# Kernel optimization log

Measured on AMD Instinct MI355X. Metric: run time of the kernel, lower is better.

## Reference

```python
import jax, jax.numpy as jnp
import numpy as np

NUM_HEADS = 4
NUM_GROUPS = 32
EPS = 1e-5


def group_norm(x, gamma, beta):
    B, C, H, W = x.shape
    g = x.reshape(B, NUM_GROUPS, C // NUM_GROUPS, H, W)
    mean = g.mean(axis=(2, 3, 4), keepdims=True)
    var = g.var(axis=(2, 3, 4), keepdims=True)
    g = (g - mean) * jax.lax.rsqrt(var + EPS)
    x = g.reshape(B, C, H, W)
    return x * gamma[None, :, None, None] + beta[None, :, None, None]


def setup_inputs() -> dict:
    key = jax.random.key(0)
    ks = jax.random.split(key, 7)
    B, C, H, W = 16, 256, 32, 32
    x = jax.random.normal(ks[0], (B, C, H, W), dtype=jnp.float32)
    gn_gamma = jnp.ones((C,), dtype=jnp.float32)
    gn_beta = jnp.zeros((C,), dtype=jnp.float32)
    s = 1.0 / np.sqrt(C)
    qkv_w = jax.random.normal(ks[1], (3 * C, C), dtype=jnp.float32) * s
    qkv_b = jnp.zeros((3 * C,), dtype=jnp.float32)
    proj_w = jax.random.normal(ks[2], (C, C), dtype=jnp.float32) * s
    proj_b = jnp.zeros((C,), dtype=jnp.float32)
    return {"x": x, "gn_gamma": gn_gamma, "gn_beta": gn_beta,
            "qkv_w": qkv_w, "qkv_b": qkv_b, "proj_w": proj_w, "proj_b": proj_b}


def reference(x, gn_gamma, gn_beta, qkv_w, qkv_b, proj_w, proj_b):
    B, C, H, W = x.shape
    nh = NUM_HEADS
    d = C // nh
    N = H * W

    h = group_norm(x, gn_gamma, gn_beta)
    # 1x1 conv == channel matmul
    qkv = jnp.einsum('bchw,oc->bohw', h, qkv_w) + qkv_b[None, :, None, None]
    qkv = qkv.reshape(B, 3, nh, d, N)
    q, k, v = qkv[:, 0], qkv[:, 1], qkv[:, 2]  # each [B, nh, d, N]

    scale = 1.0 / jnp.sqrt(jnp.asarray(d, dtype=x.dtype))
    attn = jnp.einsum('bhdn,bhdm->bhnm', q, k) * scale  # [B, nh, N, N]
    attn = jax.nn.softmax(attn, axis=-1)
    out = jnp.einsum('bhnm,bhdm->bhdn', attn, v)  # [B, nh, d, N]
    out = out.reshape(B, C, H, W)

    out = jnp.einsum('bchw,oc->bohw', out, proj_w) + proj_b[None, :, None, None]
    return x + out
```

## Files before the change

kernel.cpp:

```cpp
#include <hip/hip_runtime.h>
#include <math.h>

typedef unsigned short u16;
typedef unsigned int u32;
typedef __attribute__((ext_vector_type(8))) short s16x8;
typedef __attribute__((ext_vector_type(4))) float f32x4;

#define NB 16
#define NN 1024
#define GN_EPS 1e-5f

static __device__ __forceinline__ u16 f2bf(float f) {
    union { float f; u32 u; } v; v.f = f;
    return (u16)((v.u + 0x8000u) >> 16);
}
static __device__ __forceinline__ u32 pk2(float a, float b) {
    union { float f; u32 u; } A, B; A.f = a; B.f = b;
    return __builtin_amdgcn_perm(A.u + 0x8000u, B.u + 0x8000u, 0x03020706u);
}
static __device__ __forceinline__ u32 cvtpk2(float a, float b) {
    u32 r;
    asm("v_cvt_pk_bf16_f32 %0, %1, %2" : "=v"(r) : "v"(a), "v"(b));
    return r;
}

#define GLL16(gp, lp) __builtin_amdgcn_global_load_lds( \
    (const __attribute__((address_space(1))) void*)(const void*)(gp), \
    (__attribute__((address_space(3))) void*)(void*)(lp), 16, 0, 0)

__global__ __launch_bounds__(256) void gn_stats_kernel(
    const float* __restrict__ x, float2* __restrict__ stats)
{
    const int bg = blockIdx.x;
    const int t  = threadIdx.x;
    const float4* xb = (const float4*)(x + (size_t)bg * 8192);
    float s = 0.f, ss = 0.f;
#pragma unroll
    for (int i = 0; i < 8; ++i) {
        float4 f = xb[t + i * 256];
        s  += f.x + f.y + f.z + f.w;
        ss += f.x * f.x + f.y * f.y + f.z * f.z + f.w * f.w;
    }
#pragma unroll
    for (int off = 32; off > 0; off >>= 1) {
        s  += __shfl_down(s, off);
        ss += __shfl_down(ss, off);
    }
    __shared__ float red[8];
    const int wid = t >> 6;
    if ((t & 63) == 0) { red[wid] = s; red[4 + wid] = ss; }
    __syncthreads();
    if (t == 0) {
        float sa = red[0] + red[1] + red[2] + red[3];
        float sb = red[4] + red[5] + red[6] + red[7];
        float mean = sa * (1.0f / 8192.0f);
        float var  = sb * (1.0f / 8192.0f) - mean * mean;
        stats[bg] = make_float2(mean, 1.0f / sqrtf(var + GN_EPS));
    }
}

__global__ __launch_bounds__(256) void wcvt_kernel(
    const float* __restrict__ qkv_w, const float* __restrict__ proj_w,
    u16* __restrict__ wqb, u16* __restrict__ wpb)
{
    int i = blockIdx.x * 256 + threadIdx.x;
    if (i < 49152) {
        float4 f = ((const float4*)qkv_w)[i];
        *(uint2*)(wqb + (size_t)i * 4) = make_uint2(pk2(f.x, f.y), pk2(f.z, f.w));
    } else {
        int j = i - 49152;
        float4 f = ((const float4*)proj_w)[j];
        *(uint2*)(wpb + (size_t)j * 4) = make_uint2(pk2(f.x, f.y), pk2(f.z, f.w));
    }
}

__global__ __launch_bounds__(256) void gnorm_t_kernel(
    const float* __restrict__ x, const float2* __restrict__ stats,
    const float* __restrict__ gamma, const float* __restrict__ beta,
    u16* __restrict__ Xt)
{
    const int b = blockIdx.z, ct = blockIdx.y, nt = blockIdx.x;
    const int t = threadIdx.x;
    __shared__ float T[64][65];
    const float* xb = x + ((size_t)b * 256 + ct * 64) * NN + nt * 64;
#pragma unroll
    for (int i = 0; i < 4; ++i) {
        int row = i * 16 + (t >> 4), col = (t & 15) * 4;
        int ch = ct * 64 + row;
        float2 st = stats[b * 32 + (ch >> 3)];
        float gmv = st.y * gamma[ch];
        float btv = beta[ch] - st.x * gmv;
        float4 f = *(const float4*)&xb[(size_t)row * NN + col];
        T[row][col + 0] = f.x * gmv + btv;
        T[row][col + 1] = f.y * gmv + btv;
        T[row][col + 2] = f.z * gmv + btv;
        T[row][col + 3] = f.w * gmv + btv;
    }
    __syncthreads();
    u16* dst = Xt + ((size_t)b * NN + nt * 64) * 256 + ct * 64;
#pragma unroll
    for (int p = 0; p < 2; ++p) {
        int idx = t + p * 256;
        int nl = idx >> 3, c8 = idx & 7;
        s16x8 pv;
#pragma unroll
        for (int j = 0; j < 8; ++j) pv[j] = (short)f2bf(T[c8 * 8 + j][nl]);
        *(s16x8*)(dst + (size_t)nl * 256 + c8 * 8) = pv;
    }
}

__global__ __launch_bounds__(256, 4) void qkv_mfma_kernel(
    const u16* __restrict__ Wb, const float* __restrict__ bias,
    const u16* __restrict__ Xt,
    u16* __restrict__ qh, u16* __restrict__ kh, u16* __restrict__ vh)
{
    const int b = blockIdx.z, ot = blockIdx.y, nt = blockIdx.x;
    const int t = threadIdx.x, w = t >> 6, l = t & 63;
    const int g = l >> 4, c = l & 15;
    __shared__ u16 Slds[32 * 512];
    const u16* Xb = Xt + ((size_t)b * NN + nt * 128) * 256;

    if (ot < 4) {
        const int h = ot;
        const size_t bhoff = (size_t)(b * 4 + h) << 16;
        const u16* Wq = Wb + (size_t)(h)     * 64 * 256;
        const u16* Wk = Wb + (size_t)(4 + h) * 64 * 256;

#pragma unroll
        for (int s = w; s < 32; s += 4) {
            int osub = s >> 3, ks = s & 7;
            GLL16(Wq + (size_t)(osub * 16 + c) * 256 + ks * 32 + g * 8, Slds + s * 512);
        }
        s16x8 a0[8], a1[8];
#pragma unroll
        for (int ks = 0; ks < 8; ++ks) {
            a0[ks] = *(const s16x8*)(Xb + (size_t)((2 * w) * 16 + c) * 256 + ks * 32 + g * 8);
            a1[ks] = *(const s16x8*)(Xb + (size_t)((2 * w + 1) * 16 + c) * 256 + ks * 32 + g * 8);
        }
        f32x4 acc[2][4];
#pragma unroll
        for (int i = 0; i < 2; ++i)
#pragma unroll
            for (int j = 0; j < 4; ++j) acc[i][j] = (f32x4){0.f, 0.f, 0.f, 0.f};
        __syncthreads();
#pragma unroll
        for (int ks = 0; ks < 8; ++ks)
#pragma unroll
            for (int j = 0; j < 4; ++j) {
                s16x8 bf = *(const s16x8*)(Slds + (j * 8 + ks) * 512 + l * 8);
                acc[0][j] = __builtin_amdgcn_mfma_f32_16x16x32_bf16(a0[ks], bf, acc[0][j], 0, 0, 0);
                acc[1][j] = __builtin_amdgcn_mfma_f32_16x16x32_bf16(a1[ks], bf, acc[1][j], 0, 0, 0);
            }
        __syncthreads();

#pragma unroll
        for (int s = w; s < 32; s += 4) {
            int osub = s >> 3, ks = s & 7;
            GLL16(Wk + (size_t)(osub * 16 + c) * 256 + ks * 32 + g * 8, Slds + s * 512);
        }
        {
            const float sc = 0.125f * 1.44269504088896f;
            float bv[4];
#pragma unroll
            for (int j = 0; j < 4; ++j) bv[j] = bias[h * 64 + j * 16 + c];
            u16* dst = qh + bhoff + (size_t)(nt * 128) * 64;
#pragma unroll
            for (int i = 0; i < 2; ++i)
#pragma unroll
                for (int j = 0; j < 4; ++j)
#pragma unroll
                    for (int r = 0; r < 4; ++r) {
                        int n = (2 * w + i) * 16 + g * 4 + r;
                        dst[(size_t)n * 64 + j * 16 + c] = f2bf((acc[i][j][r] + bv[j]) * sc);
                    }
        }
#pragma unroll
        for (int i = 0; i < 2; ++i)
#pragma unroll
            for (int j = 0; j < 4; ++j) acc[i][j] = (f32x4){0.f, 0.f, 0.f, 0.f};
        asm volatile("s_waitcnt vmcnt(32)" ::: "memory");
        __builtin_amdgcn_s_barrier();
        asm volatile("" ::: "memory");
#pragma unroll
        for (int ks = 0; ks < 8; ++ks)
#pragma unroll
            for (int j = 0; j < 4; ++j) {
                s16x8 bf = *(const s16x8*)(Slds + (j * 8 + ks) * 512 + l * 8);
                acc[0][j] = __builtin_amdgcn_mfma_f32_16x16x32_bf16(a0[ks], bf, acc[0][j], 0, 0, 0);
                acc[1][j] = __builtin_amdgcn_mfma_f32_16x16x32_bf16(a1[ks], bf, acc[1][j], 0, 0, 0);
            }
        {
            float bv[4];
#pragma unroll
            for (int j = 0; j < 4; ++j) bv[j] = bias[(4 + h) * 64 + j * 16 + c];
            u16* dst = kh + bhoff + (size_t)(nt * 128) * 64;
#pragma unroll
            for (int i = 0; i < 2; ++i)
#pragma unroll
                for (int j = 0; j < 4; ++j)
#pragma unroll
                    for (int r = 0; r < 4; ++r) {
                        int n = (2 * w + i) * 16 + g * 4 + r;
                        dst[(size_t)n * 64 + j * 16 + c] = f2bf(acc[i][j][r] + bv[j]);
                    }
        }
    } else {
        const int h = ot - 4;
        const size_t bhoff = (size_t)(b * 4 + h) << 16;
        const u16* Wo = Wb + (size_t)(8 + h) * 64 * 256;
        f32x4 acc[8];
#pragma unroll
        for (int j = 0; j < 8; ++j) acc[j] = (f32x4){0.f, 0.f, 0.f, 0.f};
        for (int kk = 0; kk < 256; kk += 128) {
            if (kk) __syncthreads();
#pragma unroll
            for (int s = w; s < 32; s += 4) {
                int nsub = s >> 2, ks = s & 3;
                GLL16(Xb + (size_t)(nsub * 16 + c) * 256 + kk + ks * 32 + g * 8, Slds + s * 512);
            }
            __syncthreads();
#pragma unroll
            for (int ks = 0; ks < 4; ++ks) {
                s16x8 a = *(const s16x8*)(Wo + (size_t)(w * 16 + c) * 256 + kk + ks * 32 + g * 8);
#pragma unroll
                for (int j = 0; j < 8; ++j) {
                    s16x8 xf = *(const s16x8*)(Slds + (j * 4 + ks) * 512 + l * 8);
                    acc[j] = __builtin_amdgcn_mfma_f32_16x16x32_bf16(a, xf, acc[j], 0, 0, 0);
                }
            }
        }
        float bv[4];
#pragma unroll
        for (int r = 0; r < 4; ++r) bv[r] = bias[(8 + h) * 64 + w * 16 + g * 4 + r];
        u16* dst = vh + bhoff;
#pragma unroll
        for (int j = 0; j < 8; ++j)
#pragma unroll
            for (int r = 0; r < 4; ++r) {
                int d = w * 16 + g * 4 + r;
                int m = nt * 128 + j * 16 + c;
                dst[(size_t)d * NN + m] = f2bf(acc[j][r] + bv[r]);
            }
    }
}

__global__ __launch_bounds__(512, 4) void attn_mfma_kernel(
    const u16* __restrict__ qh, const u16* __restrict__ kh,
    const u16* __restrict__ vh, u16* __restrict__ aoT)
{
    const int t = threadIdx.x;
    const int w = t >> 6, l = t & 63;
    const int g = l >> 4, c = l & 15;
    const int bid = blockIdx.x;
    const int xcd = bid & 7;
    const int idx = bid >> 3;
    const int qt  = idx & 7;
    const int grp = (idx >> 3) * 8 + xcd;
    const int b = grp >> 2, h = grp & 3;
    const size_t bhoff = (size_t)grp << 16;
    const int n_base = qt * 128 + w * 16;

    __shared__ u16 Klds[4][8 * 512];
    __shared__ u16 Vlds[4][8 * 512];
    __shared__ u16 Plds[8][2 * 512];

    const u16* qb = qh + bhoff;
    const u16* kb = kh + bhoff;
    const u16* vb = vh + bhoff;

    const int msub = w >> 1, uu = w & 1;

    s16x8 qf[2];
#pragma unroll
    for (int u = 0; u < 2; ++u)
        qf[u] = *(const s16x8*)(qb + (size_t)(n_base + c) * 64 + u * 32 + g * 8);

    s16x8 onef;
#pragma unroll
    for (int j = 0; j < 8; ++j) onef[j] = (short)0x3F80;

    f32x4 Oacc[4];
    f32x4 Lacc = (f32x4){0.f, 0.f, 0.f, 0.f};
#pragma unroll
    for (int ds = 0; ds < 4; ++ds) Oacc[ds] = (f32x4){0.f, 0.f, 0.f, 0.f};

    u16* pw = &Plds[w][0];

#define STK(tt) GLL16(kb + (size_t)((tt) * 64 + msub * 16 + c) * 64 + uu * 32 + g * 8, &Klds[(tt) & 3][w * 512])
#define STV(tt) GLL16(vb + (size_t)(msub * 16 + c) * NN + (tt) * 64 + uu * 32 + g * 8, &Vlds[(tt) & 3][w * 512])

    auto tile = [&](int buf) {
        const u16* Kc = &Klds[buf][0];
        const u16* Vc = &Vlds[buf][0];
        f32x4 S[4];
#pragma unroll
        for (int ms = 0; ms < 4; ++ms) S[ms] = (f32x4){0.f, 0.f, 0.f, 0.f};
        __builtin_amdgcn_s_setprio(1);
#pragma unroll
        for (int ms = 0; ms < 4; ++ms)
#pragma unroll
            for (int u = 0; u < 2; ++u) {
                s16x8 af = *(const s16x8*)(Kc + (ms * 2 + u) * 512 + l * 8);
                S[ms] = __builtin_amdgcn_mfma_f32_16x16x32_bf16(af, qf[u], S[ms], 0, 0, 0);
            }
        __builtin_amdgcn_s_setprio(0);
        s16x8 vf[4][2];
#pragma unroll
        for (int ds = 0; ds < 4; ++ds)
#pragma unroll
            for (int u = 0; u < 2; ++u)
                vf[ds][u] = *(const s16x8*)(Vc + (ds * 2 + u) * 512 + l * 8);
#pragma unroll
        for (int ms = 0; ms < 4; ++ms)
#pragma unroll
            for (int r = 0; r < 4; ++r) S[ms][r] = __builtin_amdgcn_exp2f(S[ms][r]);
#pragma unroll
        for (int ms = 0; ms < 4; ++ms) {
            u32 d0 = cvtpk2(S[ms][0], S[ms][1]);
            u32 d1 = cvtpk2(S[ms][2], S[ms][3]);
            int off = (ms >> 1) * 512 + ((ms & 1) * 2 + (g >> 1)) * 128 + c * 8 + (g & 1) * 4;
            *(uint2*)(pw + off) = make_uint2(d0, d1);
        }
        __builtin_amdgcn_s_setprio(1);
#pragma unroll
        for (int u = 0; u < 2; ++u) {
            s16x8 pf = *(const s16x8*)(pw + u * 512 + l * 8);
#pragma unroll
            for (int ds = 0; ds < 4; ++ds)
                Oacc[ds] = __builtin_amdgcn_mfma_f32_16x16x32_bf16(vf[ds][u], pf, Oacc[ds], 0, 0, 0);
            Lacc = __builtin_amdgcn_mfma_f32_16x16x32_bf16(onef, pf, Lacc, 0, 0, 0);
        }
        __builtin_amdgcn_s_setprio(0);
    };

    STK(0); STV(0); STK(1); STV(1);

    for (int it = 0; it < 8; ++it) {
        if (it < 7) {
            STK(2 * it + 2); STV(2 * it + 2);
            STK(2 * it + 3); STV(2 * it + 3);
            asm volatile("s_waitcnt vmcnt(4)" ::: "memory");
        } else {
            asm volatile("s_waitcnt vmcnt(0)" ::: "memory");
        }
        __builtin_amdgcn_s_barrier();
        asm volatile("" ::: "memory");

        tile((2 * it) & 3);
        tile((2 * it + 1) & 3);

        asm volatile("" ::: "memory");
        __builtin_amdgcn_s_barrier();
    }

    u16* aob = aoT + (size_t)b * NN * 256 + h * 64;
    float inv = 1.0f / Lacc[0];
    const size_t nrow = (size_t)(n_base + c) * 256;
#pragma unroll
    for (int ds = 0; ds < 4; ++ds) {
        u32 lo = cvtpk2(Oacc[ds][0] * inv, Oacc[ds][1] * inv);
        u32 hi = cvtpk2(Oacc[ds][2] * inv, Oacc[ds][3] * inv);
        *(uint2*)(aob + nrow + ds * 16 + g * 4) = make_uint2(lo, hi);
    }
#undef STK
#undef STV
}

__global__ __launch_bounds__(256) void proj_mfma_kernel(
    const u16* __restrict__ Wb, const float* __restrict__ bias,
    const u16* __restrict__ aoT, const float* __restrict__ x,
    float* __restrict__ out)
{
    const int b = blockIdx.z, ot = blockIdx.y, nt = blockIdx.x;
    const int t = threadIdx.x, w = t >> 6, l = t & 63;
    const int g = l >> 4, c = l & 15;
    __shared__ u16 Slds[32 * 512];
    const u16* Xb = aoT + ((size_t)b * NN + nt * 128) * 256;
    const u16* Wo = Wb + (size_t)ot * 64 * 256;

    f32x4 acc[8];
#pragma unroll
    for (int j = 0; j < 8; ++j) acc[j] = (f32x4){0.f, 0.f, 0.f, 0.f};
    for (int kk = 0; kk < 256; kk += 128) {
        if (kk) __syncthreads();
#pragma unroll
        for (int s = w; s < 32; s += 4) {
            int nsub = s >> 2, ks = s & 3;
            GLL16(Xb + (size_t)(nsub * 16 + c) * 256 + kk + ks * 32 + g * 8, Slds + s * 512);
        }
        __syncthreads();
#pragma unroll
        for (int ks = 0; ks < 4; ++ks) {
            s16x8 a = *(const s16x8*)(Wo + (size_t)(w * 16 + c) * 256 + kk + ks * 32 + g * 8);
#pragma unroll
            for (int j = 0; j < 8; ++j) {
                s16x8 xf = *(const s16x8*)(Slds + (j * 4 + ks) * 512 + l * 8);
                acc[j] = __builtin_amdgcn_mfma_f32_16x16x32_bf16(a, xf, acc[j], 0, 0, 0);
            }
        }
    }
    float bv[4];
#pragma unroll
    for (int r = 0; r < 4; ++r) bv[r] = bias[ot * 64 + w * 16 + g * 4 + r];
#pragma unroll
    for (int j = 0; j < 8; ++j)
#pragma unroll
        for (int r = 0; r < 4; ++r) {
            int o = ot * 64 + w * 16 + g * 4 + r;
            int n = nt * 128 + j * 16 + c;
            size_t addr = ((size_t)b * 256 + o) * NN + n;
            out[addr] = acc[j][r] + bv[r] + x[addr];
        }
}

extern "C" void kernel_launch(void* const* d_in, const int* in_sizes, int n_in,
                              void* d_out, int out_size, void* d_ws, size_t ws_size,
                              hipStream_t stream)
{
    const float* x      = (const float*)d_in[0];
    const float* gamma  = (const float*)d_in[1];
    const float* beta   = (const float*)d_in[2];
    const float* qkv_w  = (const float*)d_in[3];
    const float* qkv_b  = (const float*)d_in[4];
    const float* proj_w = (const float*)d_in[5];
    const float* proj_b = (const float*)d_in[6];
    float* out = (float*)d_out;

    float* ws = (float*)d_ws;
    float2* stats = (float2*)ws;
    u16* Xt  = (u16*)(ws + 1024);
    u16* wqb = Xt + (size_t)4194304;
    u16* wpb = wqb + (size_t)196608;
    u16* qh  = wpb + (size_t)65536;
    u16* kh  = qh + (size_t)4194304;
    u16* vh  = kh + (size_t)4194304;
    u16* aoT = vh + (size_t)4194304;

    gn_stats_kernel<<<dim3(NB * 32), 256, 0, stream>>>(x, stats);
    wcvt_kernel<<<dim3(256), 256, 0, stream>>>(qkv_w, proj_w, wqb, wpb);
    gnorm_t_kernel<<<dim3(16, 4, NB), 256, 0, stream>>>(x, stats, gamma, beta, Xt);

    qkv_mfma_kernel<<<dim3(8, 8, NB), 256, 0, stream>>>(
        wqb, qkv_b, Xt, qh, kh, vh);

    attn_mfma_kernel<<<dim3(512), 512, 0, stream>>>(qh, kh, vh, aoT);

    proj_mfma_kernel<<<dim3(8, 4, NB), 256, 0, stream>>>(
        wpb, proj_b, aoT, x, out);
}
```

Before: 80.90 us.

## Double query rows per wave in attention to reuse K/V tiles

```diff
diff --git a/kernel.cpp b/kernel.cpp
--- a/kernel.cpp
+++ b/kernel.cpp
@@ -244,7 +244,7 @@
     }
 }
 
-__global__ __launch_bounds__(512, 4) void attn_mfma_kernel(
+__global__ __launch_bounds__(512, 2) void attn_mfma_kernel(
     const u16* __restrict__ qh, const u16* __restrict__ kh,
     const u16* __restrict__ vh, u16* __restrict__ aoT)
 {
@@ -254,15 +254,15 @@
     const int bid = blockIdx.x;
     const int xcd = bid & 7;
     const int idx = bid >> 3;
-    const int qt  = idx & 7;
-    const int grp = (idx >> 3) * 8 + xcd;
+    const int qt  = idx & 3;
+    const int grp = (idx >> 2) * 8 + xcd;
     const int b = grp >> 2, h = grp & 3;
     const size_t bhoff = (size_t)grp << 16;
-    const int n_base = qt * 128 + w * 16;
+    const int n_base = qt * 256 + w * 32;
 
     __shared__ u16 Klds[4][8 * 512];
     __shared__ u16 Vlds[4][8 * 512];
-    __shared__ u16 Plds[8][2 * 512];
+    __shared__ u16 Plds[8][4 * 512];
 
     const u16* qb = qh + bhoff;
     const u16* kb = kh + bhoff;
@@ -270,19 +270,25 @@
 
     const int msub = w >> 1, uu = w & 1;
 
-    s16x8 qf[2];
-#pragma unroll
-    for (int u = 0; u < 2; ++u)
-        qf[u] = *(const s16x8*)(qb + (size_t)(n_base + c) * 64 + u * 32 + g * 8);
+    s16x8 qf[2][2];
+#pragma unroll
+    for (int sub = 0; sub < 2; ++sub)
+#pragma unroll
+        for (int u = 0; u < 2; ++u)
+            qf[sub][u] = *(const s16x8*)(qb + (size_t)(n_base + sub * 16 + c) * 64 + u * 32 + g * 8);
 
     s16x8 onef;
 #pragma unroll
     for (int j = 0; j < 8; ++j) onef[j] = (short)0x3F80;
 
-    f32x4 Oacc[4];
-    f32x4 Lacc = (f32x4){0.f, 0.f, 0.f, 0.f};
-#pragma unroll
-    for (int ds = 0; ds < 4; ++ds) Oacc[ds] = (f32x4){0.f, 0.f, 0.f, 0.f};
+    f32x4 Oacc[2][4];
+    f32x4 Lacc[2];
+#pragma unroll
+    for (int sub = 0; sub < 2; ++sub) {
+        Lacc[sub] = (f32x4){0.f, 0.f, 0.f, 0.f};
+#pragma unroll
+        for (int ds = 0; ds < 4; ++ds) Oacc[sub][ds] = (f32x4){0.f, 0.f, 0.f, 0.f};
+    }
 
     u16* pw = &Plds[w][0];
 
@@ -292,16 +298,19 @@
     auto tile = [&](int buf) {
         const u16* Kc = &Klds[buf][0];
         const u16* Vc = &Vlds[buf][0];
-        f32x4 S[4];
-#pragma unroll
-        for (int ms = 0; ms < 4; ++ms) S[ms] = (f32x4){0.f, 0.f, 0.f, 0.f};
+        f32x4 S[2][4];
+#pragma unroll
+        for (int sub = 0; sub < 2; ++sub)
+#pragma unroll
+            for (int ms = 0; ms < 4; ++ms) S[sub][ms] = (f32x4){0.f, 0.f, 0.f, 0.f};
         __builtin_amdgcn_s_setprio(1);
 #pragma unroll
         for (int ms = 0; ms < 4; ++ms)
 #pragma unroll
             for (int u = 0; u < 2; ++u) {
                 s16x8 af = *(const s16x8*)(Kc + (ms * 2 + u) * 512 + l * 8);
-                S[ms] = __builtin_amdgcn_mfma_f32_16x16x32_bf16(af, qf[u], S[ms], 0, 0, 0);
+                S[0][ms] = __builtin_amdgcn_mfma_f32_16x16x32_bf16(af, qf[0][u], S[0][ms], 0, 0, 0);
+                S[1][ms] = __builtin_amdgcn_mfma_f32_16x16x32_bf16(af, qf[1][u], S[1][ms], 0, 0, 0);
             }
         __builtin_amdgcn_s_setprio(0);
         s16x8 vf[4][2];
@@ -311,25 +320,31 @@
             for (int u = 0; u < 2; ++u)
                 vf[ds][u] = *(const s16x8*)(Vc + (ds * 2 + u) * 512 + l * 8);
 #pragma unroll
-        for (int ms = 0; ms < 4; ++ms)
-#pragma unroll
-            for (int r = 0; r < 4; ++r) S[ms][r] = __builtin_amdgcn_exp2f(S[ms][r]);
-#pragma unroll
-        for (int ms = 0; ms < 4; ++ms) {
-            u32 d0 = cvtpk2(S[ms][0], S[ms][1]);
-            u32 d1 = cvtpk2(S[ms][2], S[ms][3]);
-            int off = (ms >> 1) * 512 + ((ms & 1) * 2 + (g >> 1)) * 128 + c * 8 + (g & 1) * 4;
-            *(uint2*)(pw + off) = make_uint2(d0, d1);
-        }
+        for (int sub = 0; sub < 2; ++sub)
+#pragma unroll
+            for (int ms = 0; ms < 4; ++ms)
+#pragma unroll
+                for (int r = 0; r < 4; ++r) S[sub][ms][r] = __builtin_amdgcn_exp2f(S[sub][ms][r]);
+#pragma unroll
+        for (int sub = 0; sub < 2; ++sub)
+#pragma unroll
+            for (int ms = 0; ms < 4; ++ms) {
+                u32 d0 = cvtpk2(S[sub][ms][0], S[sub][ms][1]);
+                u32 d1 = cvtpk2(S[sub][ms][2], S[sub][ms][3]);
+                int off = (sub * 2 + (ms >> 1)) * 512 + ((ms & 1) * 2 + (g >> 1)) * 128 + c * 8 + (g & 1) * 4;
+                *(uint2*)(pw + off) = make_uint2(d0, d1);
+            }
         __builtin_amdgcn_s_setprio(1);
 #pragma unroll
-        for (int u = 0; u < 2; ++u) {
-            s16x8 pf = *(const s16x8*)(pw + u * 512 + l * 8);
-#pragma unroll
-            for (int ds = 0; ds < 4; ++ds)
-                Oacc[ds] = __builtin_amdgcn_mfma_f32_16x16x32_bf16(vf[ds][u], pf, Oacc[ds], 0, 0, 0);
-            Lacc = __builtin_amdgcn_mfma_f32_16x16x32_bf16(onef, pf, Lacc, 0, 0, 0);
-        }
+        for (int sub = 0; sub < 2; ++sub)
+#pragma unroll
+            for (int u = 0; u < 2; ++u) {
+                s16x8 pf = *(const s16x8*)(pw + (sub * 2 + u) * 512 + l * 8);
+#pragma unroll
+                for (int ds = 0; ds < 4; ++ds)
+                    Oacc[sub][ds] = __builtin_amdgcn_mfma_f32_16x16x32_bf16(vf[ds][u], pf, Oacc[sub][ds], 0, 0, 0);
+                Lacc[sub] = __builtin_amdgcn_mfma_f32_16x16x32_bf16(onef, pf, Lacc[sub], 0, 0, 0);
+            }
         __builtin_amdgcn_s_setprio(0);
     };
 
@@ -354,13 +369,16 @@
     }
 
     u16* aob = aoT + (size_t)b * NN * 256 + h * 64;
-    float inv = 1.0f / Lacc[0];
-    const size_t nrow = (size_t)(n_base + c) * 256;
-#pragma unroll
-    for (int ds = 0; ds < 4; ++ds) {
-        u32 lo = cvtpk2(Oacc[ds][0] * inv, Oacc[ds][1] * inv);
-        u32 hi = cvtpk2(Oacc[ds][2] * inv, Oacc[ds][3] * inv);
-        *(uint2*)(aob + nrow + ds * 16 + g * 4) = make_uint2(lo, hi);
+#pragma unroll
+    for (int sub = 0; sub < 2; ++sub) {
+        float inv = 1.0f / Lacc[sub][0];
+        const size_t nrow = (size_t)(n_base + sub * 16 + c) * 256;
+#pragma unroll
+        for (int ds = 0; ds < 4; ++ds) {
+            u32 lo = cvtpk2(Oacc[sub][ds][0] * inv, Oacc[sub][ds][1] * inv);
+            u32 hi = cvtpk2(Oacc[sub][ds][2] * inv, Oacc[sub][ds][3] * inv);
+            *(uint2*)(aob + nrow + ds * 16 + g * 4) = make_uint2(lo, hi);
+        }
     }
 #undef STK
 #undef STV
@@ -443,7 +461,7 @@
     qkv_mfma_kernel<<<dim3(8, 8, NB), 256, 0, stream>>>(
         wqb, qkv_b, Xt, qh, kh, vh);
 
-    attn_mfma_kernel<<<dim3(512), 512, 0, stream>>>(qh, kh, vh, aoT);
+    attn_mfma_kernel<<<dim3(256), 512, 0, stream>>>(qh, kh, vh, aoT);
 
     proj_mfma_kernel<<<dim3(8, 4, NB), 256, 0, stream>>>(
         wpb, proj_b, aoT, x, out);
```

Result: slower. 82.68 us (+2.2%).

## Fuse group-norm stats and normalize into one kernel with grouped layout

Applied to the files above, without the earlier changes.

```diff
diff --git a/kernel.cpp b/kernel.cpp
--- a/kernel.cpp
+++ b/kernel.cpp
@@ -28,16 +28,23 @@
     (const __attribute__((address_space(1))) void*)(const void*)(gp), \
     (__attribute__((address_space(3))) void*)(void*)(lp), 16, 0, 0)
 
-__global__ __launch_bounds__(256) void gn_stats_kernel(
-    const float* __restrict__ x, float2* __restrict__ stats)
-{
-    const int bg = blockIdx.x;
+__global__ __launch_bounds__(256) void gn_fused_kernel(
+    const float* __restrict__ x, const float* __restrict__ gamma,
+    const float* __restrict__ beta, u16* __restrict__ Xtg)
+{
+    const int gg = blockIdx.x;
+    const int b  = blockIdx.y;
     const int t  = threadIdx.x;
-    const float4* xb = (const float4*)(x + (size_t)bg * 8192);
+    __shared__ float T[8 * 1028];
+    __shared__ float red[8];
+    __shared__ float sstat[2];
+
+    const float4* xb = (const float4*)(x + ((size_t)b * 32 + gg) * 8192);
     float s = 0.f, ss = 0.f;
 #pragma unroll
     for (int i = 0; i < 8; ++i) {
-        float4 f = xb[t + i * 256];
+        float4 f = xb[i * 256 + t];
+        *(float4*)&T[i * 1028 + t * 4] = f;
         s  += f.x + f.y + f.z + f.w;
         ss += f.x * f.x + f.y * f.y + f.z * f.z + f.w * f.w;
     }
@@ -46,16 +53,36 @@
         s  += __shfl_down(s, off);
         ss += __shfl_down(ss, off);
     }
-    __shared__ float red[8];
-    const int wid = t >> 6;
-    if ((t & 63) == 0) { red[wid] = s; red[4 + wid] = ss; }
+    if ((t & 63) == 0) { red[t >> 6] = s; red[4 + (t >> 6)] = ss; }
     __syncthreads();
     if (t == 0) {
         float sa = red[0] + red[1] + red[2] + red[3];
         float sb = red[4] + red[5] + red[6] + red[7];
         float mean = sa * (1.0f / 8192.0f);
         float var  = sb * (1.0f / 8192.0f) - mean * mean;
-        stats[bg] = make_float2(mean, 1.0f / sqrtf(var + GN_EPS));
+        sstat[0] = mean; sstat[1] = 1.0f / sqrtf(var + GN_EPS);
+    }
+    __syncthreads();
+    const float mean = sstat[0], rstd = sstat[1];
+    float gm[8], bt[8];
+#pragma unroll
+    for (int j = 0; j < 8; ++j) {
+        float gj = gamma[gg * 8 + j];
+        gm[j] = gj * rstd;
+        bt[j] = beta[gg * 8 + j] - mean * rstd * gj;
+    }
+    u16* dst = Xtg + ((size_t)(b * 32 + gg) * NN) * 8;
+#pragma unroll
+    for (int rep = 0; rep < 4; ++rep) {
+        int n = rep * 256 + t;
+        u32 o[4];
+#pragma unroll
+        for (int p = 0; p < 4; ++p) {
+            float v0 = T[(2 * p)     * 1028 + n] * gm[2 * p]     + bt[2 * p];
+            float v1 = T[(2 * p + 1) * 1028 + n] * gm[2 * p + 1] + bt[2 * p + 1];
+            o[p] = pk2(v0, v1);
+        }
+        *(uint4*)(dst + (size_t)n * 8) = make_uint4(o[0], o[1], o[2], o[3]);
     }
 }
 
@@ -74,51 +101,16 @@
     }
 }
 
-__global__ __launch_bounds__(256) void gnorm_t_kernel(
-    const float* __restrict__ x, const float2* __restrict__ stats,
-    const float* __restrict__ gamma, const float* __restrict__ beta,
-    u16* __restrict__ Xt)
-{
-    const int b = blockIdx.z, ct = blockIdx.y, nt = blockIdx.x;
-    const int t = threadIdx.x;
-    __shared__ float T[64][65];
-    const float* xb = x + ((size_t)b * 256 + ct * 64) * NN + nt * 64;
-#pragma unroll
-    for (int i = 0; i < 4; ++i) {
-        int row = i * 16 + (t >> 4), col = (t & 15) * 4;
-        int ch = ct * 64 + row;
-        float2 st = stats[b * 32 + (ch >> 3)];
-        float gmv = st.y * gamma[ch];
-        float btv = beta[ch] - st.x * gmv;
-        float4 f = *(const float4*)&xb[(size_t)row * NN + col];
-        T[row][col + 0] = f.x * gmv + btv;
-        T[row][col + 1] = f.y * gmv + btv;
-        T[row][col + 2] = f.z * gmv + btv;
-        T[row][col + 3] = f.w * gmv + btv;
-    }
-    __syncthreads();
-    u16* dst = Xt + ((size_t)b * NN + nt * 64) * 256 + ct * 64;
-#pragma unroll
-    for (int p = 0; p < 2; ++p) {
-        int idx = t + p * 256;
-        int nl = idx >> 3, c8 = idx & 7;
-        s16x8 pv;
-#pragma unroll
-        for (int j = 0; j < 8; ++j) pv[j] = (short)f2bf(T[c8 * 8 + j][nl]);
-        *(s16x8*)(dst + (size_t)nl * 256 + c8 * 8) = pv;
-    }
-}
-
 __global__ __launch_bounds__(256, 4) void qkv_mfma_kernel(
     const u16* __restrict__ Wb, const float* __restrict__ bias,
-    const u16* __restrict__ Xt,
+    const u16* __restrict__ Xtg,
     u16* __restrict__ qh, u16* __restrict__ kh, u16* __restrict__ vh)
 {
     const int b = blockIdx.z, ot = blockIdx.y, nt = blockIdx.x;
     const int t = threadIdx.x, w = t >> 6, l = t & 63;
     const int g = l >> 4, c = l & 15;
     __shared__ u16 Slds[32 * 512];
-    const u16* Xb = Xt + ((size_t)b * NN + nt * 128) * 256;
+    const u16* Xb = Xtg + (size_t)b * 32 * NN * 8;
 
     if (ot < 4) {
         const int h = ot;
@@ -134,8 +126,8 @@
         s16x8 a0[8], a1[8];
 #pragma unroll
         for (int ks = 0; ks < 8; ++ks) {
-            a0[ks] = *(const s16x8*)(Xb + (size_t)((2 * w) * 16 + c) * 256 + ks * 32 + g * 8);
-            a1[ks] = *(const s16x8*)(Xb + (size_t)((2 * w + 1) * 16 + c) * 256 + ks * 32 + g * 8);
+            a0[ks] = *(const s16x8*)(Xb + ((size_t)(ks * 4 + g) * NN + nt * 128 + (2 * w) * 16 + c) * 8);
+            a1[ks] = *(const s16x8*)(Xb + ((size_t)(ks * 4 + g) * NN + nt * 128 + (2 * w + 1) * 16 + c) * 8);
         }
         f32x4 acc[2][4];
 #pragma unroll
@@ -216,7 +208,7 @@
 #pragma unroll
             for (int s = w; s < 32; s += 4) {
                 int nsub = s >> 2, ks = s & 3;
-                GLL16(Xb + (size_t)(nsub * 16 + c) * 256 + kk + ks * 32 + g * 8, Slds + s * 512);
+                GLL16(Xb + ((size_t)((kk >> 3) + ks * 4 + g) * NN + nt * 128 + nsub * 16 + c) * 8, Slds + s * 512);
             }
             __syncthreads();
 #pragma unroll
@@ -427,21 +419,19 @@
     float* out = (float*)d_out;
 
     float* ws = (float*)d_ws;
-    float2* stats = (float2*)ws;
-    u16* Xt  = (u16*)(ws + 1024);
-    u16* wqb = Xt + (size_t)4194304;
+    u16* Xtg = (u16*)(ws + 1024);
+    u16* wqb = Xtg + (size_t)4194304;
     u16* wpb = wqb + (size_t)196608;
     u16* qh  = wpb + (size_t)65536;
     u16* kh  = qh + (size_t)4194304;
     u16* vh  = kh + (size_t)4194304;
     u16* aoT = vh + (size_t)4194304;
 
-    gn_stats_kernel<<<dim3(NB * 32), 256, 0, stream>>>(x, stats);
     wcvt_kernel<<<dim3(256), 256, 0, stream>>>(qkv_w, proj_w, wqb, wpb);
-    gnorm_t_kernel<<<dim3(16, 4, NB), 256, 0, stream>>>(x, stats, gamma, beta, Xt);
+    gn_fused_kernel<<<dim3(32, NB), 256, 0, stream>>>(x, gamma, beta, Xtg);
 
     qkv_mfma_kernel<<<dim3(8, 8, NB), 256, 0, stream>>>(
-        wqb, qkv_b, Xt, qh, kh, vh);
+        wqb, qkv_b, Xtg, qh, kh, vh);
 
     attn_mfma_kernel<<<dim3(512), 512, 0, stream>>>(qh, kh, vh, aoT);
 
```

Result: faster. 74.10 us (-8.4%).
